# Performance work log

Measured on AMD Instinct MI355X. Metric: run time of the kernel, lower is better.

Reference implementation:

```python
import jax, jax.numpy as jnp
import numpy as np

B, S, P, D, H = 2, 1024, 1024, 2048, 16
HD = D // H  # 128
T = P + S


def setup_inputs() -> dict:
    key = jax.random.key(0)
    ks = jax.random.split(key, 12)
    hidden_state = jax.random.normal(ks[0], (B, S, D), dtype=jnp.float32)
    past_key = jax.random.normal(ks[1], (B, H, P, HD), dtype=jnp.float32)
    past_value = jax.random.normal(ks[2], (B, H, P, HD), dtype=jnp.float32)
    # causal mask: query i sits at global position P+i; mask (1.0) keys j > P+i
    rows = P + jnp.arange(S)[:, None]
    cols = jnp.arange(T)[None, :]
    casual_mask = (cols > rows).astype(jnp.float32)[None, None]  # [1,1,S,T]
    # pad mask: mask out the last 128 key positions
    pad_mask = jnp.zeros((B, T), dtype=jnp.float32).at[:, T - 128:].set(1.0)
    init = lambda k, shp: (jax.random.normal(k, shp, dtype=jnp.float32) * 0.02)
    Wq, bq = init(ks[3], (D, D)), init(ks[4], (D,))
    Wk, bk = init(ks[5], (D, D)), init(ks[6], (D,))
    Wv, bv = init(ks[7], (D, D)), init(ks[8], (D,))
    Wo, bo = init(ks[9], (D, D)), init(ks[10], (D,))
    return dict(hidden_state=hidden_state, past_key=past_key, past_value=past_value,
                casual_mask=casual_mask, pad_mask=pad_mask,
                Wq=Wq, bq=bq, Wk=Wk, bk=bk, Wv=Wv, bv=bv, Wo=Wo, bo=bo)


def _split_heads(x):
    b, s, _ = x.shape
    return x.reshape(b, s, H, HD).transpose(0, 2, 1, 3)  # [B,H,S,HD]


def reference(hidden_state, past_key, past_value, casual_mask, pad_mask,
              Wq, bq, Wk, bk, Wv, bv, Wo, bo):
    q = _split_heads(jnp.einsum('bsd,ed->bse', hidden_state, Wq) + bq)
    k = _split_heads(jnp.einsum('bsd,ed->bse', hidden_state, Wk) + bk)
    v = _split_heads(jnp.einsum('bsd,ed->bse', hidden_state, Wv) + bv)
    k = jnp.concatenate([past_key, k], axis=2)   # [B,H,T,HD]
    v = jnp.concatenate([past_value, v], axis=2)
    scale = jnp.sqrt(jnp.float32(HD))
    scores = jnp.einsum('bhqd,bhkd->bhqk', q, k) / scale
    scores = scores + casual_mask * -1e9 + pad_mask[:, None, None, :] * -1e9
    probs = jax.nn.softmax(scores, axis=-1)
    out = jnp.einsum('bhqk,bhkd->bhqd', probs, v)
    out = out.transpose(0, 2, 1, 3).reshape(hidden_state.shape[0], -1, D)
    output = jnp.einsum('bsd,ed->bse', out, Wo) + bo
    # use_cache=True in original returns (output, (k, v)); return flat tuple
    return output, k, v
```

## Files before the change

### kernel.cpp

```cpp
#include <hip/hip_runtime.h>
#include <stdint.h>

typedef unsigned short u16t;
using bf16x8 = __attribute__((ext_vector_type(8))) short;
using f32x4  = __attribute__((ext_vector_type(4))) float;
using u16x8  = __attribute__((ext_vector_type(8))) unsigned short;
using u32x4  = __attribute__((ext_vector_type(4))) unsigned int;
using fl4    = __attribute__((ext_vector_type(4))) float;

#define DEVI static __device__ __forceinline__

DEVI u16t f2bf(float x) {
    union { float f; unsigned u; } v; v.f = x;
    return (u16t)((v.u + 0x7fffu + ((v.u >> 16) & 1u)) >> 16);
}

#define GLL16(gp, lp) __builtin_amdgcn_global_load_lds( \
    (const __attribute__((address_space(1))) void*)(gp), \
    (__attribute__((address_space(3))) void*)(lp), 16, 0, 0)

DEVI f32x4 mfma16(bf16x8 a, bf16x8 b, f32x4 c) {
    return __builtin_amdgcn_mfma_f32_16x16x32_bf16(a, b, c, 0, 0, 0);
}

DEVI unsigned cvt_pk_bf16(float lo, float hi) {
    unsigned r;
    asm("v_cvt_pk_bf16_f32 %0, %1, %2" : "=v"(r) : "v"(lo), "v"(hi));
    return r;
}

__global__ void k_f2bf5(const float* __restrict__ h,  const float* __restrict__ wq,
                        const float* __restrict__ wk, const float* __restrict__ wv,
                        const float* __restrict__ wo, u16t* __restrict__ xb,
                        u16t* __restrict__ wb) {
    const float* src = h;  u16t* dst = xb;
    int which = blockIdx.y;
    if      (which == 1) { src = wq; dst = wb; }
    else if (which == 2) { src = wk; dst = wb + 4194304; }
    else if (which == 3) { src = wv; dst = wb + 8388608; }
    else if (which == 4) { src = wo; dst = wb + 12582912; }
    size_t i = (size_t)blockIdx.x * blockDim.x + threadIdx.x;
    const fl4* s = (const fl4*)(src + i * 8);
    fl4 a = s[0], b = s[1];
    u16x8 o;
    o[0]=f2bf(a[0]); o[1]=f2bf(a[1]); o[2]=f2bf(a[2]); o[3]=f2bf(a[3]);
    o[4]=f2bf(b[0]); o[5]=f2bf(b[1]); o[6]=f2bf(b[2]); o[7]=f2bf(b[3]);
    *(u16x8*)(dst + i * 8) = o;
}

__global__ void k_copy_past2(const float* __restrict__ pk, const float* __restrict__ pv,
                             u16t* __restrict__ Kb, u16t* __restrict__ Vb,
                             float* __restrict__ kout, float* __restrict__ vout) {
    const float* src = pk; u16t* dstb = Kb; float* dstf = kout;
    if (blockIdx.y == 1) { src = pv; dstb = Vb; dstf = vout; }
    size_t i = (size_t)blockIdx.x * blockDim.x + threadIdx.x;
    int bh = (int)(i >> 14);
    int r  = (int)(i & 16383);
    const fl4* s = (const fl4*)(src + i * 8);
    fl4 a = s[0], b = s[1];
    size_t dof = (size_t)bh * 262144 + (size_t)r * 8;
    *(fl4*)(dstf + dof) = a;
    *(fl4*)(dstf + dof + 4) = b;
    u16x8 o;
    o[0]=f2bf(a[0]); o[1]=f2bf(a[1]); o[2]=f2bf(a[2]); o[3]=f2bf(a[3]);
    o[4]=f2bf(b[0]); o[5]=f2bf(b[1]); o[6]=f2bf(b[2]); o[7]=f2bf(b[3]);
    *(u16x8*)(dstb + dof) = o;
}

__global__ void k_transpose_v(const u16t* __restrict__ Vb, u16t* __restrict__ Vtb) {
    __shared__ u16t tile[64 * 72];
    int bh  = blockIdx.z;
    int t0  = blockIdx.x * 64;
    int hd0 = blockIdx.y * 64;
    int tid = threadIdx.x;
    #pragma unroll
    for (int p = 0; p < 2; ++p) {
        int c = tid + p * 256;
        int tl = c >> 3, c8 = (c & 7) * 8;
        u16x8 v = *(const u16x8*)(Vb + ((size_t)bh * 2048 + t0 + tl) * 128 + hd0 + c8);
        *(u16x8*)(tile + tl * 72 + c8) = v;
    }
    __syncthreads();
    #pragma unroll
    for (int p = 0; p < 2; ++p) {
        int c = tid + p * 256;
        int hl = c >> 3, t8 = (c & 7) * 8;
        u16x8 v;
        #pragma unroll
        for (int j = 0; j < 8; ++j) v[j] = tile[(t8 + j) * 72 + hl];
        *(u16x8*)(Vtb + ((size_t)bh * 128 + hd0 + hl) * 2048 + t0 + t8) = v;
    }
}

template <int EPI>
__global__ void k_gemm(const u16t* __restrict__ A, const u16t* __restrict__ B,
                       const float* __restrict__ b0, const float* __restrict__ b1,
                       const float* __restrict__ b2,
                       u16t* __restrict__ Qb, u16t* __restrict__ Kb, u16t* __restrict__ Vb,
                       float* __restrict__ kout, float* __restrict__ vout,
                       float* __restrict__ outF) {
    __shared__ u16t As[128 * 64];
    __shared__ u16t Bs[128 * 64];
    const int tid  = threadIdx.x;
    const int lane = tid & 63;
    const int w    = tid >> 6;
    const int wm = w >> 1, wn = w & 1;
    const int m0 = blockIdx.x * 128;
    const int n0 = blockIdx.y * 128;
    const int srow = lane >> 3;
    const int scol = (lane & 7) * 8;
    const int fr = lane & 15, fg = lane >> 4;

    f32x4 acc[4][4] = {};

    const u16t* Ag = A + (size_t)(m0 + srow) * 2048 + scol;
    const u16t* Bg = B + (size_t)(n0 + srow) * 2048 + scol;

    for (int k0 = 0; k0 < 2048; k0 += 64) {
        #pragma unroll
        for (int j = 0; j < 4; ++j) {
            int is = w * 4 + j;
            GLL16(Ag + (size_t)is * 8 * 2048 + k0, As + is * 512);
            GLL16(Bg + (size_t)is * 8 * 2048 + k0, Bs + is * 512);
        }
        __syncthreads();
        bf16x8 af[2][4], bfr[2][4];
        #pragma unroll
        for (int m = 0; m < 4; ++m) {
            af[0][m] = *(const bf16x8*)(As + (wm * 64 + m * 16 + fr) * 64 + fg * 8);
            af[1][m] = *(const bf16x8*)(As + (wm * 64 + m * 16 + fr) * 64 + 32 + fg * 8);
        }
        #pragma unroll
        for (int n = 0; n < 4; ++n) {
            bfr[0][n] = *(const bf16x8*)(Bs + (wn * 64 + n * 16 + fr) * 64 + fg * 8);
            bfr[1][n] = *(const bf16x8*)(Bs + (wn * 64 + n * 16 + fr) * 64 + 32 + fg * 8);
        }
        #pragma unroll
        for (int kk = 0; kk < 2; ++kk)
            #pragma unroll
            for (int m = 0; m < 4; ++m)
                #pragma unroll
                for (int n = 0; n < 4; ++n)
                    acc[m][n] = mfma16(af[kk][m], bfr[kk][n], acc[m][n]);
        __syncthreads();
    }

    if (EPI == 0) {
        #pragma unroll
        for (int n = 0; n < 4; ++n) {
            int c = n0 + wn * 64 + n * 16 + fr;
            float bias = b0[c];
            #pragma unroll
            for (int m = 0; m < 4; ++m) {
                int r = m0 + wm * 64 + m * 16 + fg * 4;
                #pragma unroll
                for (int rr = 0; rr < 4; ++rr)
                    outF[(size_t)(r + rr) * 2048 + c] = acc[m][n][rr] + bias;
            }
        }
    } else {
        int group = n0 >> 11;
        const float* bias = (group == 0) ? b0 : (group == 1 ? b1 : b2);
        #pragma unroll
        for (int n = 0; n < 4; ++n) {
            int c = n0 + wn * 64 + n * 16 + fr;
            int e = c & 2047;
            int h = e >> 7, hd = e & 127;
            float bv = bias[e];
            #pragma unroll
            for (int m = 0; m < 4; ++m) {
                int r = m0 + wm * 64 + m * 16 + fg * 4;
                #pragma unroll
                for (int rr = 0; rr < 4; ++rr) {
                    int rg = r + rr;
                    int b = rg >> 10, s = rg & 1023;
                    float v = acc[m][n][rr] + bv;
                    if (group == 0) {
                        Qb[(((size_t)b * 16 + h) * 1024 + s) * 128 + hd] = f2bf(v);
                    } else {
                        size_t idx = (((size_t)b * 16 + h) * 2048 + 1024 + s) * 128 + hd;
                        if (group == 1) { Kb[idx] = f2bf(v); kout[idx] = v; }
                        else            { Vb[idx] = f2bf(v); vout[idx] = v; }
                    }
                }
            }
        }
    }
}

__global__ void k_flash(const u16t* __restrict__ Qb, const u16t* __restrict__ Kb,
                        const u16t* __restrict__ Vtb, u16t* __restrict__ Ao) {
    __shared__ u16t Ks[2][64 * 128];
    __shared__ u16t Vs[2][128 * 64];
    const int tid = threadIdx.x;
    const int lane = tid & 63;
    const int w = tid >> 6;
    const int bh = blockIdx.x;
    const int q0 = blockIdx.y * 64;
    const int fr = lane & 15, fg = lane >> 4;

    bf16x8 qf[4];
    {
        const u16t* qp = Qb + ((size_t)bh * 1024 + q0 + w * 16 + fr) * 128 + fg * 8;
        #pragma unroll
        for (int kk = 0; kk < 4; ++kk) qf[kk] = *(const bf16x8*)(qp + kk * 32);
    }

    f32x4 acc[8] = {};
    float m_r = -1e30f, l_r = 0.0f;

    const int ntiles = min((1024 + q0 + 63) / 64 + 1, 30);

    const int krow_s = lane >> 4;
    const int koff_s = (lane & 15) * 8;
    const int vrow_s = lane >> 3;
    const int vc = (lane & 7) ^ (lane >> 3);
    const int vperm8 = ((vc & 4) | ((vc & 1) << 1) | ((vc >> 1) & 1)) * 8;
    const int qpos = 1024 + q0 + w * 16 + fr;

    const u16t* Kg = Kb  + (size_t)bh * 262144;
    const u16t* Vg = Vtb + (size_t)bh * 262144;

#define STAGE(tt, bb) do {                                                        \
    int j0s = (tt) * 64;                                                          \
    _Pragma("unroll")                                                             \
    for (int j = 0; j < 4; ++j) {                                                 \
        int is = w * 4 + j;                                                       \
        int kr = is * 4 + krow_s;                                                 \
        GLL16(Kg + (size_t)(j0s + kr) * 128 + (koff_s ^ ((kr & 7) << 3)),         \
              &Ks[bb][is * 512]);                                                 \
        int vr = is * 8 + vrow_s;                                                 \
        GLL16(Vg + (size_t)vr * 2048 + j0s + vperm8, &Vs[bb][is * 512]);          \
    }                                                                             \
} while (0)

    int cur = 0;
    STAGE(0, 0);
    __syncthreads();

    const float scale = 0.08838834764831845f;
    const float L2E = 1.4426950408889634f;

    for (int t = 0; t < ntiles; ++t) {
        if (t + 1 < ntiles) STAGE(t + 1, cur ^ 1);
        const int j0 = t * 64;
        const u16t* kb = &Ks[cur][0];
        const u16t* vb = &Vs[cur][0];

        f32x4 sc[4] = {};
        #pragma unroll
        for (int kt = 0; kt < 4; ++kt) {
            int krow = kt * 16 + fr;
            int sw = (krow & 7) << 3;
            #pragma unroll
            for (int kk = 0; kk < 4; ++kk) {
                bf16x8 kf = *(const bf16x8*)(kb + krow * 128 + ((kk * 32 + fg * 8) ^ sw));
                sc[kt] = mfma16(kf, qf[kk], sc[kt]);
            }
        }

        float pp[4][4];
        float mt = -3e30f;
        if (j0 + 63 > 1024 + q0 + w * 16) {
            #pragma unroll
            for (int kt = 0; kt < 4; ++kt)
                #pragma unroll
                for (int rr = 0; rr < 4; ++rr) {
                    float v = sc[kt][rr] * scale;
                    int jk = j0 + kt * 16 + fg * 4 + rr;
                    if (jk > qpos) v = -3e30f;
                    pp[kt][rr] = v;
                    mt = fmaxf(mt, v);
                }
        } else {
            #pragma unroll
            for (int kt = 0; kt < 4; ++kt)
                #pragma unroll
                for (int rr = 0; rr < 4; ++rr) {
                    float v = sc[kt][rr] * scale;
                    pp[kt][rr] = v;
                    mt = fmaxf(mt, v);
                }
        }
        mt = fmaxf(mt, __shfl_xor(mt, 16));
        mt = fmaxf(mt, __shfl_xor(mt, 32));
        float mn = fmaxf(m_r, mt);
        float cf = exp2f((m_r - mn) * L2E);
        m_r = mn;
        float ls = 0.0f;
        #pragma unroll
        for (int kt = 0; kt < 4; ++kt)
            #pragma unroll
            for (int rr = 0; rr < 4; ++rr) {
                float p = exp2f((pp[kt][rr] - mn) * L2E);
                pp[kt][rr] = p;
                ls += p;
            }
        ls += __shfl_xor(ls, 16);
        ls += __shfl_xor(ls, 32);
        l_r = l_r * cf + ls;

        unsigned wp[4][2];
        #pragma unroll
        for (int kt = 0; kt < 4; ++kt) {
            wp[kt][0] = cvt_pk_bf16(pp[kt][0], pp[kt][1]);
            wp[kt][1] = cvt_pk_bf16(pp[kt][2], pp[kt][3]);
        }
        const bool fodd = (fg & 1) != 0;
        unsigned X0 = fodd ? wp[0][0] : wp[1][0];
        unsigned X1 = fodd ? wp[0][1] : wp[1][1];
        unsigned X2 = fodd ? wp[2][0] : wp[3][0];
        unsigned X3 = fodd ? wp[2][1] : wp[3][1];
        unsigned Y0 = (unsigned)__shfl_xor((int)X0, 16);
        unsigned Y1 = (unsigned)__shfl_xor((int)X1, 16);
        unsigned Y2 = (unsigned)__shfl_xor((int)X2, 16);
        unsigned Y3 = (unsigned)__shfl_xor((int)X3, 16);

        float cfo[4];
        #pragma unroll
        for (int rr = 0; rr < 4; ++rr) cfo[rr] = __shfl(cf, fg * 4 + rr);
        #pragma unroll
        for (int cg = 0; cg < 8; ++cg)
            #pragma unroll
            for (int rr = 0; rr < 4; ++rr)
                acc[cg][rr] *= cfo[rr];

        u32x4 a0v, a1v;
        if (!fodd) {
            a0v[0] = wp[0][0]; a0v[1] = wp[0][1]; a0v[2] = Y0; a0v[3] = Y1;
            a1v[0] = wp[2][0]; a1v[1] = wp[2][1]; a1v[2] = Y2; a1v[3] = Y3;
        } else {
            a0v[0] = Y0; a0v[1] = Y1; a0v[2] = wp[1][0]; a0v[3] = wp[1][1];
            a1v[0] = Y2; a1v[1] = Y3; a1v[2] = wp[3][0]; a1v[3] = wp[3][1];
        }
        bf16x8 pa0 = __builtin_bit_cast(bf16x8, a0v);
        bf16x8 pa1 = __builtin_bit_cast(bf16x8, a1v);

        #pragma unroll
        for (int kk = 0; kk < 2; ++kk) {
            bf16x8 pa = kk ? pa1 : pa0;
            #pragma unroll
            for (int cg = 0; cg < 8; ++cg) {
                int vrow = cg * 16 + fr;
                bf16x8 vf = *(const bf16x8*)(vb + vrow * 64 +
                                             ((fg * 8 + kk * 32) ^ ((vrow & 7) << 3)));
                acc[cg] = mfma16(pa, vf, acc[cg]);
            }
        }
        __syncthreads();
        cur ^= 1;
    }
#undef STAGE

    float linv[4];
    #pragma unroll
    for (int rr = 0; rr < 4; ++rr) linv[rr] = 1.0f / __shfl(l_r, fg * 4 + rr);
    const int b = bh >> 4, h = bh & 15;
    const int sbase = q0 + w * 16 + fg * 4;
    #pragma unroll
    for (int cg = 0; cg < 8; ++cg) {
        #pragma unroll
        for (int rr = 0; rr < 4; ++rr) {
            size_t idx = ((size_t)b * 1024 + sbase + rr) * 2048 + h * 128 + cg * 16 + fr;
            Ao[idx] = f2bf(acc[cg][rr] * linv[rr]);
        }
    }
}

extern "C" void kernel_launch(void* const* d_in, const int* in_sizes, int n_in,
                              void* d_out, int out_size, void* d_ws, size_t ws_size,
                              hipStream_t stream) {
    const float* hidden = (const float*)d_in[0];
    const float* pkey   = (const float*)d_in[1];
    const float* pval   = (const float*)d_in[2];
    const float* Wq = (const float*)d_in[5];
    const float* bq = (const float*)d_in[6];
    const float* Wk = (const float*)d_in[7];
    const float* bk = (const float*)d_in[8];
    const float* Wv = (const float*)d_in[9];
    const float* bv = (const float*)d_in[10];
    const float* Wo = (const float*)d_in[11];
    const float* bo = (const float*)d_in[12];

    float* outp = (float*)d_out;
    float* kout = outp + 4194304;
    float* vout = outp + 12582912;

    char* ws = (char*)d_ws;
    u16t* Xb  = (u16t*)(ws);
    u16t* Wb  = (u16t*)(ws + (size_t)8  * 1048576);
    u16t* Qb  = (u16t*)(ws + (size_t)40 * 1048576);
    u16t* Kb  = (u16t*)(ws + (size_t)48 * 1048576);
    u16t* Vb  = (u16t*)(ws + (size_t)64 * 1048576);
    u16t* Vtb = (u16t*)(ws + (size_t)80 * 1048576);
    u16t* Ao  = Xb;
    if (ws_size < (size_t)96 * 1048576) return;

    k_f2bf5<<<dim3(2048, 5), 256, 0, stream>>>(hidden, Wq, Wk, Wv, Wo, Xb, Wb);
    k_copy_past2<<<dim3(2048, 2), 256, 0, stream>>>(pkey, pval, Kb, Vb, kout, vout);
    k_gemm<1><<<dim3(16, 48), 256, 0, stream>>>(Xb, Wb, bq, bk, bv,
                                                Qb, Kb, Vb, kout, vout, nullptr);
    k_transpose_v<<<dim3(32, 2, 32), 256, 0, stream>>>(Vb, Vtb);
    k_flash<<<dim3(32, 16), 256, 0, stream>>>(Qb, Kb, Vtb, Ao);
    k_gemm<0><<<dim3(16, 16), 256, 0, stream>>>(Ao, Wb + 12582912, bo, nullptr, nullptr,
                                                nullptr, nullptr, nullptr, nullptr, nullptr, outp);
}
```

Measured before the change: 387.4 us.

## Double-buffer LDS tiles in GEMM to overlap global loads with MFMA

```diff
diff --git a/kernel.cpp b/kernel.cpp
--- a/kernel.cpp
+++ b/kernel.cpp
@@ -99,8 +99,8 @@
                        u16t* __restrict__ Qb, u16t* __restrict__ Kb, u16t* __restrict__ Vb,
                        float* __restrict__ kout, float* __restrict__ vout,
                        float* __restrict__ outF) {
-    __shared__ u16t As[128 * 64];
-    __shared__ u16t Bs[128 * 64];
+    __shared__ u16t As[2][128 * 64];
+    __shared__ u16t Bs[2][128 * 64];
     const int tid  = threadIdx.x;
     const int lane = tid & 63;
     const int w    = tid >> 6;
@@ -116,24 +116,33 @@
     const u16t* Ag = A + (size_t)(m0 + srow) * 2048 + scol;
     const u16t* Bg = B + (size_t)(n0 + srow) * 2048 + scol;
 
-    for (int k0 = 0; k0 < 2048; k0 += 64) {
-        #pragma unroll
-        for (int j = 0; j < 4; ++j) {
-            int is = w * 4 + j;
-            GLL16(Ag + (size_t)is * 8 * 2048 + k0, As + is * 512);
-            GLL16(Bg + (size_t)is * 8 * 2048 + k0, Bs + is * 512);
-        }
-        __syncthreads();
+#define GSTAGE(k0s, bb) do {                                                \
+    _Pragma("unroll")                                                       \
+    for (int j = 0; j < 4; ++j) {                                           \
+        int is = w * 4 + j;                                                 \
+        GLL16(Ag + (size_t)is * 8 * 2048 + (k0s), &As[bb][is * 512]);       \
+        GLL16(Bg + (size_t)is * 8 * 2048 + (k0s), &Bs[bb][is * 512]);       \
+    }                                                                       \
+} while (0)
+
+    int cur = 0;
+    GSTAGE(0, 0);
+    __syncthreads();
+
+    for (int t = 0; t < 32; ++t) {
+        if (t + 1 < 32) GSTAGE((t + 1) * 64, cur ^ 1);
+        const u16t* as = &As[cur][0];
+        const u16t* bs = &Bs[cur][0];
         bf16x8 af[2][4], bfr[2][4];
         #pragma unroll
         for (int m = 0; m < 4; ++m) {
-            af[0][m] = *(const bf16x8*)(As + (wm * 64 + m * 16 + fr) * 64 + fg * 8);
-            af[1][m] = *(const bf16x8*)(As + (wm * 64 + m * 16 + fr) * 64 + 32 + fg * 8);
+            af[0][m] = *(const bf16x8*)(as + (wm * 64 + m * 16 + fr) * 64 + fg * 8);
+            af[1][m] = *(const bf16x8*)(as + (wm * 64 + m * 16 + fr) * 64 + 32 + fg * 8);
         }
         #pragma unroll
         for (int n = 0; n < 4; ++n) {
-            bfr[0][n] = *(const bf16x8*)(Bs + (wn * 64 + n * 16 + fr) * 64 + fg * 8);
-            bfr[1][n] = *(const bf16x8*)(Bs + (wn * 64 + n * 16 + fr) * 64 + 32 + fg * 8);
+            bfr[0][n] = *(const bf16x8*)(bs + (wn * 64 + n * 16 + fr) * 64 + fg * 8);
+            bfr[1][n] = *(const bf16x8*)(bs + (wn * 64 + n * 16 + fr) * 64 + 32 + fg * 8);
         }
         #pragma unroll
         for (int kk = 0; kk < 2; ++kk)
@@ -143,7 +152,9 @@
                 for (int n = 0; n < 4; ++n)
                     acc[m][n] = mfma16(af[kk][m], bfr[kk][n], acc[m][n]);
         __syncthreads();
-    }
+        cur ^= 1;
+    }
+#undef GSTAGE
 
     if (EPI == 0) {
         #pragma unroll
```

Result: slower. 441.6 us (+14.0%).
